# Kernel tuning notes

Measured on AMD Instinct MI355X. Metric: run time of the kernel, lower is better.

Reference implementation:

```python
import jax, jax.numpy as jnp
import numpy as np

N_HEAD, D_MODEL, D_HEAD = 16, 1024, 64
SCALE = 1.0 / (D_HEAD ** 0.5)
LN_EPS = 1e-5


def _rel_shift(x):
    # x: [b, n, i, j] -> Transformer-XL relative shift
    b, n, i, j = x.shape
    x_padded = jnp.pad(x, ((0, 0), (0, 0), (0, 0), (1, 0)))  # [b,n,i,j+1]
    x_padded = x_padded.reshape(b, n, j + 1, i)
    return x_padded[:, :, 1:, :].reshape(b, n, i, j)


def _layer_norm(x, g, b):
    mu = jnp.mean(x, axis=-1, keepdims=True)
    var = jnp.mean(jnp.square(x - mu), axis=-1, keepdims=True)
    return (x - mu) * jax.lax.rsqrt(var + LN_EPS) * g + b


def setup_inputs() -> dict:
    key = jax.random.key(0)
    ks = jax.random.split(key, 16)
    qlen, bsz = 2048, 2
    d = D_MODEL
    h = N_HEAD * D_HEAD
    s = 0.02
    inp = {
        "w": jax.random.normal(ks[0], (qlen, bsz, d), jnp.float32),
        "r": jax.random.normal(ks[1], (qlen, d), jnp.float32),
        "r_w_bias": jax.random.normal(ks[2], (N_HEAD, D_HEAD), jnp.float32) * s,
        "r_r_bias": jax.random.normal(ks[3], (N_HEAD, D_HEAD), jnp.float32) * s,
        "Wq": jax.random.normal(ks[4], (d, h), jnp.float32) * s,
        "bq": jnp.zeros((h,), jnp.float32),
        "Wk": jax.random.normal(ks[5], (d, h), jnp.float32) * s,
        "bk": jnp.zeros((h,), jnp.float32),
        "Wv": jax.random.normal(ks[6], (d, h), jnp.float32) * s,
        "bv": jnp.zeros((h,), jnp.float32),
        "Wr": jax.random.normal(ks[7], (d, h), jnp.float32) * s,
        "br": jnp.zeros((h,), jnp.float32),
        "Wo": jax.random.normal(ks[8], (h, d), jnp.float32) * s,
        "bo": jnp.zeros((d,), jnp.float32),
        "ln_g": jnp.ones((d,), jnp.float32),
        "ln_b": jnp.zeros((d,), jnp.float32),
        # causal mask: True = masked (future positions)
        "attn_mask": jnp.triu(jnp.ones((qlen, qlen), dtype=bool), k=1),
    }
    return inp


def reference(w, r, r_w_bias, r_r_bias, Wq, bq, Wk, bk, Wv, bv, Wr, br, Wo, bo, ln_g, ln_b, attn_mask):
    qlen, bsz, _ = w.shape
    rlen = r.shape[0]
    # projections (post-lnorm path: project raw w)
    q = (w @ Wq + bq).reshape(qlen, bsz, N_HEAD, D_HEAD)
    k = (w @ Wk + bk).reshape(qlen, bsz, N_HEAD, D_HEAD)
    v = (w @ Wv + bv).reshape(qlen, bsz, N_HEAD, D_HEAD)
    r_k = (r @ Wr + br).reshape(rlen, N_HEAD, D_HEAD)

    AC = jnp.einsum('ibnd,jbnd->bnij', q + r_w_bias, k)
    BD = jnp.einsum('ibnd,jnd->bnij', q + r_r_bias, r_k)
    BD = _rel_shift(BD)
    attn_score = SCALE * (AC + BD)
    attn_score = jnp.where(attn_mask[None, None, :, :], -jnp.inf, attn_score)

    attn_prob = jax.nn.softmax(attn_score, axis=3)
    attn_vec = jnp.einsum('bnij,jbnd->ibnd', attn_prob, v)
    attn_vec = attn_vec.reshape(qlen, bsz, N_HEAD * D_HEAD)
    attn_out = attn_vec @ Wo + bo
    return _layer_norm(w + attn_out, ln_g, ln_b)
```

## Files before the change

kernel.cpp:

```cpp
#include <hip/hip_runtime.h>
#include <math.h>

#define L 2048
#define BSZ 2
#define NH 16
#define DH 64
#define DM 1024
#define GK 1024
#define SCALE_F 0.125f

#define PSLOT 4160

typedef __attribute__((ext_vector_type(8))) __bf16 bf16x8;
typedef __attribute__((ext_vector_type(4))) __bf16 bf16x4;
typedef __attribute__((ext_vector_type(4))) float f32x4;

__global__ __launch_bounds__(256)
void cast2_f32_bf16(const float* __restrict__ a, int na4,
                    const float* __restrict__ b, int nb4,
                    __bf16* __restrict__ da, __bf16* __restrict__ db_)
{
    int i = blockIdx.x * 256 + threadIdx.x;
    int stride = gridDim.x * 256;
    int tot = na4 + nb4;
    for (; i < tot; i += stride) {
        const float4* s; bf16x4* d; int idx;
        if (i < na4) { s = (const float4*)a; d = (bf16x4*)da; idx = i; }
        else         { s = (const float4*)b; d = (bf16x4*)db_; idx = i - na4; }
        float4 v = s[idx];
        bf16x4 o = { (__bf16)v.x, (__bf16)v.y, (__bf16)v.z, (__bf16)v.w };
        d[idx] = o;
    }
}

__global__ __launch_bounds__(256)
void transpose_w5(const float* s0, const float* s1, const float* s2,
                  const float* s3, const float* s4,
                  __bf16* d0, __bf16* d1, __bf16* d2, __bf16* d3, __bf16* d4)
{
    const float* srcs[5] = { s0, s1, s2, s3, s4 };
    __bf16*      dsts[5] = { d0, d1, d2, d3, d4 };
    const float* src = srcs[blockIdx.z];
    __bf16*      dst = dsts[blockIdx.z];
    __shared__ float tile[32][33];
    const int tx = threadIdx.x & 31, ty = threadIdx.x >> 5;
    const int x0 = blockIdx.x * 32, y0 = blockIdx.y * 32;
    #pragma unroll
    for (int i = 0; i < 32; i += 8)
        tile[ty + i][tx] = src[(size_t)(y0 + ty + i) * 1024 + x0 + tx];
    __syncthreads();
    #pragma unroll
    for (int i = 0; i < 32; i += 8)
        dst[(size_t)(x0 + ty + i) * 1024 + y0 + tx] = (__bf16)tile[tx][ty + i];
}

__global__ __launch_bounds__(256)
void transpose_v(const __bf16* __restrict__ src, __bf16* __restrict__ dst)
{
    __shared__ __bf16 tile[32][34];
    const __bf16* s = src + (size_t)blockIdx.z * L * DH;
    __bf16*       d = dst + (size_t)blockIdx.z * L * DH;
    const int tx = threadIdx.x & 31, ty = threadIdx.x >> 5;
    const int j0 = blockIdx.x * 32, d0 = blockIdx.y * 32;
    #pragma unroll
    for (int i = 0; i < 32; i += 8)
        tile[ty + i][tx] = s[(size_t)(j0 + ty + i) * DH + d0 + tx];
    __syncthreads();
    #pragma unroll
    for (int i = 0; i < 32; i += 8)
        d[(size_t)(d0 + ty + i) * L + j0 + tx] = tile[tx][ty + i];
}

__global__ __launch_bounds__(256)
void gemm_bf16(const __bf16* __restrict__ A0, const __bf16* __restrict__ A1,
               const __bf16* __restrict__ B0, const __bf16* __restrict__ B1,
               int sched,
               __bf16* __restrict__ o0, __bf16* __restrict__ o1,
               __bf16* __restrict__ o2, __bf16* __restrict__ o3,
               __bf16* __restrict__ o4,
               const float* __restrict__ b0, const float* __restrict__ b1,
               const float* __restrict__ b2, const float* __restrict__ b3,
               const float* __restrict__ rwbf, const float* __restrict__ rrbf,
               float* __restrict__ of)
{
    __shared__ __bf16 As[128 * 64];
    __shared__ __bf16 Bs[128 * 64];

    const __bf16 *A, *Bt;
    int mode, bm, bn;
    if (sched == 0) {
        int id = blockIdx.x;
        if (id < 768) { A = A0; Bt = B0; mode = 0; bm = (id & 31) * 128; bn = (id >> 5) * 128; }
        else { id -= 768; A = A1; Bt = B1; mode = 1; bm = (id & 15) * 128; bn = (id >> 4) * 128; }
    } else {
        A = A0; Bt = B0; mode = 2; bm = blockIdx.x * 128; bn = blockIdx.y * 128;
    }

    const int t    = threadIdx.x;
    const int w    = t >> 6;
    const int lane = t & 63;
    const int row16 = lane & 15;
    const int kgrp  = lane >> 4;
    const int wr = w >> 1, wc = w & 1;

    f32x4 acc[4][4];
    #pragma unroll
    for (int mi = 0; mi < 4; ++mi)
        #pragma unroll
        for (int ni = 0; ni < 4; ++ni)
            acc[mi][ni] = (f32x4){0.f, 0.f, 0.f, 0.f};

    for (int k0 = 0; k0 < GK; k0 += 64) {
        __syncthreads();
        #pragma unroll
        for (int it = 0; it < 4; ++it) {
            const int lin = (it * 256 + t) * 16;
            const int row = lin >> 7;
            const int kb  = lin & 127;
            const char* ga = (const char*)(A + (size_t)(bm + row) * GK + k0) + kb;
            __builtin_amdgcn_global_load_lds(
                (const __attribute__((address_space(1))) void*)ga,
                (__attribute__((address_space(3))) void*)((char*)As + lin), 16, 0, 0);
            const char* gb = (const char*)(Bt + (size_t)(bn + row) * GK + k0) + kb;
            __builtin_amdgcn_global_load_lds(
                (const __attribute__((address_space(1))) void*)gb,
                (__attribute__((address_space(3))) void*)((char*)Bs + lin), 16, 0, 0);
        }
        __syncthreads();

        #pragma unroll
        for (int ks = 0; ks < 2; ++ks) {
            bf16x8 af[4], bfr[4];
            #pragma unroll
            for (int mi = 0; mi < 4; ++mi)
                af[mi] = *reinterpret_cast<const bf16x8*>(
                    &As[(wr * 64 + mi * 16 + row16) * 64 + kgrp * 8 + ks * 32]);
            #pragma unroll
            for (int ni = 0; ni < 4; ++ni)
                bfr[ni] = *reinterpret_cast<const bf16x8*>(
                    &Bs[(wc * 64 + ni * 16 + row16) * 64 + kgrp * 8 + ks * 32]);
            #pragma unroll
            for (int mi = 0; mi < 4; ++mi)
                #pragma unroll
                for (int ni = 0; ni < 4; ++ni)
                    acc[mi][ni] = __builtin_amdgcn_mfma_f32_16x16x32_bf16(
                        af[mi], bfr[ni], acc[mi][ni], 0, 0, 0);
        }
    }

    #pragma unroll
    for (int mi = 0; mi < 4; ++mi) {
        #pragma unroll
        for (int ni = 0; ni < 4; ++ni) {
            #pragma unroll
            for (int r = 0; r < 4; ++r) {
                const int row = bm + wr * 64 + mi * 16 + kgrp * 4 + r;
                const int col = bn + wc * 64 + ni * 16 + row16;
                const float val = acc[mi][ni][r];
                if (mode == 0) {
                    const int which = col >> 10, c = col & 1023;
                    const int n = c >> 6, dh = c & 63;
                    const int i = row >> 1, b = row & 1;
                    const size_t idx = (((size_t)(b * NH + n) * L) + i) * DH + dh;
                    if (which == 0) {
                        const float v0 = val + b0[c];
                        o0[idx] = (__bf16)(v0 + rwbf[c]);
                        o1[idx] = (__bf16)(v0 + rrbf[c]);
                    } else if (which == 1) {
                        o2[idx] = (__bf16)(val + b1[c]);
                    } else {
                        o3[idx] = (__bf16)(val + b2[c]);
                    }
                } else if (mode == 1) {
                    const int n = col >> 6, dh = col & 63;
                    o4[((size_t)n * L + row) * DH + dh] = (__bf16)(val + b3[col]);
                } else {
                    of[(size_t)row * DM + col] = val + b0[col];
                }
            }
        }
    }
}

__global__ __launch_bounds__(256, 3)
void attn_partial(const __bf16* __restrict__ qwg, const __bf16* __restrict__ qrg,
                  const __bf16* __restrict__ kg,  const __bf16* __restrict__ vTg,
                  const __bf16* __restrict__ rkg, float* __restrict__ P)
{
    __shared__ __bf16 kt [2][64][72];
    __shared__ __bf16 vtT[2][64][72];
    __shared__ __bf16 pt [4][16][72];

    int x = blockIdx.x;
    int it, jc;
    if (x < 8)       { it = x;                      jc = 0; }
    else if (x < 24) { int y = x - 8;  it = 8  + (y >> 1); jc = y & 1; }
    else if (x < 48) { int y = x - 24; it = 16 + y / 3;    jc = y - (y / 3) * 3; }
    else             { int y = x - 48; it = 24 + (y >> 2); jc = y & 3; }

    const int t    = threadIdx.x;
    const int w    = t >> 6;
    const int lane = t & 63;
    const int row16 = lane & 15;
    const int kgrp  = lane >> 4;

    const int bh = blockIdx.y;
    const int n  = bh & (NH - 1);
    const int i0 = it * 64;
    const int i0w = i0 + w * 16;
    const int jstart = jc * 512;
    const int jend   = min(jstart + 512, i0 + 64);

    const __bf16* qwb = qwg + (size_t)bh * L * DH;
    const __bf16* qrb = qrg + (size_t)bh * L * DH;
    const __bf16* kb  = kg  + (size_t)bh * L * DH;
    const __bf16* vTb = vTg + (size_t)bh * L * DH;
    const __bf16* rkb = rkg + (size_t)n  * L * DH;

    bf16x8 qwf[2], qrf[2];
    #pragma unroll
    for (int ks = 0; ks < 2; ++ks) {
        size_t off = (size_t)(i0w + row16) * DH + kgrp * 8 + ks * 32;
        qwf[ks] = *reinterpret_cast<const bf16x8*>(qwb + off);
        qrf[ks] = *reinterpret_cast<const bf16x8*>(qrb + off);
    }

    const int sj = t >> 2;
    const int sc = (t & 3) * 16;

    {
        bf16x8 a0 = *reinterpret_cast<const bf16x8*>(kb + (size_t)(jstart + sj) * DH + sc);
        bf16x8 a1 = *reinterpret_cast<const bf16x8*>(kb + (size_t)(jstart + sj) * DH + sc + 8);
        bf16x8 b0v = *reinterpret_cast<const bf16x8*>(vTb + (size_t)sj * L + jstart + sc);
        bf16x8 b1v = *reinterpret_cast<const bf16x8*>(vTb + (size_t)sj * L + jstart + sc + 8);
        *reinterpret_cast<bf16x8*>(&kt[0][sj][sc])      = a0;
        *reinterpret_cast<bf16x8*>(&kt[0][sj][sc + 8])  = a1;
        *reinterpret_cast<bf16x8*>(&vtT[0][sj][sc])     = b0v;
        *reinterpret_cast<bf16x8*>(&vtT[0][sj][sc + 8]) = b1v;
    }
    __syncthreads();

    float l_run[4] = {0.f, 0.f, 0.f, 0.f};
    f32x4 O[4];
    #pragma unroll
    for (int cb = 0; cb < 4; ++cb) O[cb] = (f32x4){0.f, 0.f, 0.f, 0.f};

    int cur = 0;
    for (int j0 = jstart; j0 < jend; j0 += 64) {
        const bool more = (j0 + 64 < jend);

        bf16x8 skA, skB, svA, svB;
        if (more) {
            skA = *reinterpret_cast<const bf16x8*>(kb + (size_t)(j0 + 64 + sj) * DH + sc);
            skB = *reinterpret_cast<const bf16x8*>(kb + (size_t)(j0 + 64 + sj) * DH + sc + 8);
            svA = *reinterpret_cast<const bf16x8*>(vTb + (size_t)sj * L + j0 + 64 + sc);
            svB = *reinterpret_cast<const bf16x8*>(vTb + (size_t)sj * L + j0 + 64 + sc + 8);
        }

        f32x4 ac[4];
        #pragma unroll
        for (int cb = 0; cb < 4; ++cb) ac[cb] = (f32x4){0.f, 0.f, 0.f, 0.f};
        #pragma unroll
        for (int ks = 0; ks < 2; ++ks)
            #pragma unroll
            for (int cb = 0; cb < 4; ++cb) {
                bf16x8 kf = *reinterpret_cast<const bf16x8*>(
                    &kt[cur][16 * cb + row16][kgrp * 8 + ks * 32]);
                ac[cb] = __builtin_amdgcn_mfma_f32_16x16x32_bf16(qwf[ks], kf, ac[cb], 0, 0, 0);
            }

        f32x4 db[5];
        #pragma unroll
        for (int cb = 0; cb < 5; ++cb) db[cb] = (f32x4){0.f, 0.f, 0.f, 0.f};
        const int pw0 = (L - 1) + j0 - (i0w + 15);
        #pragma unroll
        for (int ks = 0; ks < 2; ++ks)
            #pragma unroll
            for (int cb = 0; cb < 5; ++cb) {
                int p = pw0 + 16 * cb + row16;
                p = p > (L - 1) ? (L - 1) : p;
                bf16x8 rf = *reinterpret_cast<const bf16x8*>(
                    rkb + (size_t)p * DH + kgrp * 8 + ks * 32);
                db[cb] = __builtin_amdgcn_mfma_f32_16x16x32_bf16(qrf[ks], rf, db[cb], 0, 0, 0);
            }

        #pragma unroll
        for (int r = 0; r < 4; ++r) {
            const int ri = kgrp * 4 + r;
            const int i_glob = i0w + ri;
            const int u  = row16 + 15 - ri;
            const int lo = u & 15;
            const int hi = u >> 4;
            const int srclane = (lane & 48) | lo;
            float T[5];
            #pragma unroll
            for (int c2 = 0; c2 < 5; ++c2)
                T[c2] = __shfl(db[c2][r], srclane, 64);
            float rsum = 0.f;
            #pragma unroll
            for (int cb = 0; cb < 4; ++cb) {
                const int jj = 16 * cb + row16;
                float bd = hi ? T[cb + 1] : T[cb];
                float s = SCALE_F * (ac[cb][r] + bd);
                if (j0 + jj > i_glob) s = -INFINITY;
                float p = __expf(s);
                pt[w][ri][jj] = (__bf16)p;
                rsum += p;
            }
            #pragma unroll
            for (int off = 1; off < 16; off <<= 1)
                rsum += __shfl_xor(rsum, off);
            l_run[r] += rsum;
        }

        #pragma unroll
        for (int ks = 0; ks < 2; ++ks) {
            bf16x8 pf = *reinterpret_cast<const bf16x8*>(&pt[w][row16][kgrp * 8 + ks * 32]);
            #pragma unroll
            for (int cb = 0; cb < 4; ++cb) {
                bf16x8 vf = *reinterpret_cast<const bf16x8*>(
                    &vtT[cur][16 * cb + row16][kgrp * 8 + ks * 32]);
                O[cb] = __builtin_amdgcn_mfma_f32_16x16x32_bf16(pf, vf, O[cb], 0, 0, 0);
            }
        }

        if (more) {
            *reinterpret_cast<bf16x8*>(&kt[cur ^ 1][sj][sc])      = skA;
            *reinterpret_cast<bf16x8*>(&kt[cur ^ 1][sj][sc + 8])  = skB;
            *reinterpret_cast<bf16x8*>(&vtT[cur ^ 1][sj][sc])     = svA;
            *reinterpret_cast<bf16x8*>(&vtT[cur ^ 1][sj][sc + 8]) = svB;
            __syncthreads();
            cur ^= 1;
        }
    }

    float* Pb = P + ((size_t)bh * 32 + it) * PSLOT;
    #pragma unroll
    for (int r = 0; r < 4; ++r) {
        const int row = w * 16 + kgrp * 4 + r;
        #pragma unroll
        for (int cb = 0; cb < 4; ++cb)
            atomicAdd(&Pb[row * 64 + 16 * cb + row16], O[cb][r]);
        if (row16 == 0)
            atomicAdd(&Pb[4096 + row], l_run[r]);
    }
}

__global__ __launch_bounds__(256)
void attn_reduce(const float* __restrict__ P, __bf16* __restrict__ av)
{
    const int bh = blockIdx.y;
    const int it = blockIdx.x;
    const int n = bh & (NH - 1), b = bh >> 4;
    const float* Pb = P + ((size_t)bh * 32 + it) * PSLOT;
    const int t = threadIdx.x;
    const int row = t >> 2;
    const int c0 = (t & 3) * 16;
    const float inv = 1.0f / Pb[4096 + row];
    const int i_glob = it * 64 + row;
    __bf16* dst = av + (size_t)(i_glob * BSZ + b) * (NH * DH) + n * DH + c0;
    #pragma unroll
    for (int v4 = 0; v4 < 4; ++v4) {
        float4 o = *reinterpret_cast<const float4*>(&Pb[row * 64 + c0 + v4 * 4]);
        bf16x4 ov = { (__bf16)(o.x * inv), (__bf16)(o.y * inv),
                      (__bf16)(o.z * inv), (__bf16)(o.w * inv) };
        *reinterpret_cast<bf16x4*>(dst + v4 * 4) = ov;
    }
}

__global__ __launch_bounds__(256)
void ln_fused(const float* __restrict__ w, const float* __restrict__ ao,
              const float* __restrict__ g, const float* __restrict__ bb,
              float* __restrict__ out)
{
    const int row = blockIdx.x;
    const float* wr = w  + (size_t)row * DM;
    const float* ar = ao + (size_t)row * DM;
    const int t = threadIdx.x;
    float x[4];
    float s = 0.f;
    #pragma unroll
    for (int j = 0; j < 4; ++j) {
        int c = t + j * 256;
        x[j] = wr[c] + ar[c];
        s += x[j];
    }
    __shared__ float red[4];
    #pragma unroll
    for (int off = 1; off < 64; off <<= 1) s += __shfl_xor(s, off);
    int wid = t >> 6, lane = t & 63;
    if (lane == 0) red[wid] = s;
    __syncthreads();
    float mu = (red[0] + red[1] + red[2] + red[3]) * (1.0f / DM);
    float ss = 0.f;
    #pragma unroll
    for (int j = 0; j < 4; ++j) { float d = x[j] - mu; ss += d * d; }
    #pragma unroll
    for (int off = 1; off < 64; off <<= 1) ss += __shfl_xor(ss, off);
    __syncthreads();
    if (lane == 0) red[wid] = ss;
    __syncthreads();
    float var = (red[0] + red[1] + red[2] + red[3]) * (1.0f / DM);
    float rstd = rsqrtf(var + 1e-5f);
    #pragma unroll
    for (int j = 0; j < 4; ++j) {
        int c = t + j * 256;
        out[(size_t)row * DM + c] = (x[j] - mu) * rstd * g[c] + bb[c];
    }
}

extern "C" void kernel_launch(void* const* d_in, const int* in_sizes, int n_in,
                              void* d_out, int out_size, void* d_ws, size_t ws_size,
                              hipStream_t stream)
{
    (void)in_sizes; (void)n_in; (void)out_size; (void)ws_size;
    const float* w   = (const float*)d_in[0];
    const float* r   = (const float*)d_in[1];
    const float* rwb = (const float*)d_in[2];
    const float* rrb = (const float*)d_in[3];
    const float* Wq  = (const float*)d_in[4];
    const float* bq  = (const float*)d_in[5];
    const float* Wk  = (const float*)d_in[6];
    const float* bk  = (const float*)d_in[7];
    const float* Wv  = (const float*)d_in[8];
    const float* bv  = (const float*)d_in[9];
    const float* Wr  = (const float*)d_in[10];
    const float* br  = (const float*)d_in[11];
    const float* Wo  = (const float*)d_in[12];
    const float* bo  = (const float*)d_in[13];
    const float* lng = (const float*)d_in[14];
    const float* lnb = (const float*)d_in[15];
    float* out = (float*)d_out;

    const size_t NQ = (size_t)BSZ * NH * L * DH;
    const size_t PN = (size_t)BSZ * NH * 32 * PSLOT;
    char* wsb = (char*)d_ws;
    __bf16* w_bf    = (__bf16*)wsb;  wsb += (size_t)2 * L * DM * 2;
    __bf16* r_bf    = (__bf16*)wsb;  wsb += (size_t)L * DM * 2;
    __bf16* wqkv_t  = (__bf16*)wsb;  wsb += (size_t)3 * DM * DM * 2;
    __bf16* wr_t    = (__bf16*)wsb;  wsb += (size_t)DM * DM * 2;
    __bf16* wo_t    = (__bf16*)wsb;  wsb += (size_t)DM * DM * 2;
    __bf16* qw_ws   = (__bf16*)wsb;  wsb += NQ * 2;
    __bf16* qr_ws   = (__bf16*)wsb;  wsb += NQ * 2;
    __bf16* k_ws    = (__bf16*)wsb;  wsb += NQ * 2;
    __bf16* v_ws    = (__bf16*)wsb;  wsb += NQ * 2;
    __bf16* vT_ws   = (__bf16*)wsb;  wsb += NQ * 2;
    __bf16* rk_ws   = (__bf16*)wsb;  wsb += (size_t)NH * L * DH * 2;
    __bf16* av_ws   = (__bf16*)wsb;  wsb += NQ * 2;
    float*  P_ws    = (float*)wsb;
    float*  ao_ws   = P_ws;

    dim3 blk(256);
    hipMemsetAsync(P_ws, 0, PN * sizeof(float), stream);

    cast2_f32_bf16<<<dim3(1536), blk, 0, stream>>>(
        w, (2 * L * DM) / 4, r, (L * DM) / 4, w_bf, r_bf);
    transpose_w5<<<dim3(32, 32, 5), blk, 0, stream>>>(
        Wq, Wk, Wv, Wr, Wo,
        wqkv_t, wqkv_t + (size_t)DM * DM, wqkv_t + (size_t)2 * DM * DM, wr_t, wo_t);

    gemm_bf16<<<dim3(896), blk, 0, stream>>>(w_bf, r_bf, wqkv_t, wr_t, 0,
        qw_ws, qr_ws, k_ws, v_ws, rk_ws, bq, bk, bv, br, rwb, rrb, nullptr);

    transpose_v<<<dim3(L / 32, DH / 32, BSZ * NH), blk, 0, stream>>>(v_ws, vT_ws);

    attn_partial<<<dim3(80, BSZ * NH), blk, 0, stream>>>(
        qw_ws, qr_ws, k_ws, vT_ws, rk_ws, P_ws);
    attn_reduce<<<dim3(32, BSZ * NH), blk, 0, stream>>>(P_ws, av_ws);

    gemm_bf16<<<dim3(32, 8), blk, 0, stream>>>(av_ws, nullptr, wo_t, nullptr, 1,
        nullptr, nullptr, nullptr, nullptr, nullptr, bo, nullptr, nullptr, nullptr,
        nullptr, nullptr, ao_ws);

    ln_fused<<<dim3(L * BSZ), blk, 0, stream>>>(w, ao_ws, lng, lnb, out);
}
```

Measured before the change: 407.4 us.

## Replace atomic partial accumulation with per-chunk bf16 slots and prefetch rel-pos keys

```diff
diff --git a/kernel.cpp b/kernel.cpp
--- a/kernel.cpp
+++ b/kernel.cpp
@@ -8,8 +8,6 @@
 #define DM 1024
 #define GK 1024
 #define SCALE_F 0.125f
-
-#define PSLOT 4160
 
 typedef __attribute__((ext_vector_type(8))) __bf16 bf16x8;
 typedef __attribute__((ext_vector_type(4))) __bf16 bf16x4;
@@ -185,18 +183,22 @@
 __global__ __launch_bounds__(256, 3)
 void attn_partial(const __bf16* __restrict__ qwg, const __bf16* __restrict__ qrg,
                   const __bf16* __restrict__ kg,  const __bf16* __restrict__ vTg,
-                  const __bf16* __restrict__ rkg, float* __restrict__ P)
+                  const __bf16* __restrict__ rkg,
+                  __bf16* __restrict__ Po, float* __restrict__ Pl)
 {
     __shared__ __bf16 kt [2][64][72];
     __shared__ __bf16 vtT[2][64][72];
     __shared__ __bf16 pt [4][16][72];
 
-    int x = blockIdx.x;
+    const int flat = blockIdx.x;
+    const int xr = flat & 7, q = flat >> 3;
+    const int bh = xr * 4 + (q / 80);
+    const int cx = 79 - (q % 80);
     int it, jc;
-    if (x < 8)       { it = x;                      jc = 0; }
-    else if (x < 24) { int y = x - 8;  it = 8  + (y >> 1); jc = y & 1; }
-    else if (x < 48) { int y = x - 24; it = 16 + y / 3;    jc = y - (y / 3) * 3; }
-    else             { int y = x - 48; it = 24 + (y >> 2); jc = y & 3; }
+    if (cx < 8)       { it = cx;                       jc = 0; }
+    else if (cx < 24) { int y = cx - 8;  it = 8  + (y >> 1); jc = y & 1; }
+    else if (cx < 48) { int y = cx - 24; it = 16 + y / 3;    jc = y - (y / 3) * 3; }
+    else              { int y = cx - 48; it = 24 + (y >> 2); jc = y & 3; }
 
     const int t    = threadIdx.x;
     const int w    = t >> 6;
@@ -204,7 +206,6 @@
     const int row16 = lane & 15;
     const int kgrp  = lane >> 4;
 
-    const int bh = blockIdx.y;
     const int n  = bh & (NH - 1);
     const int i0 = it * 64;
     const int i0w = i0 + w * 16;
@@ -238,6 +239,19 @@
         *reinterpret_cast<bf16x8*>(&vtT[0][sj][sc])     = b0v;
         *reinterpret_cast<bf16x8*>(&vtT[0][sj][sc + 8]) = b1v;
     }
+    bf16x8 rfc[2][5];
+    {
+        const int pw0 = (L - 1) + jstart - (i0w + 15);
+        #pragma unroll
+        for (int ks = 0; ks < 2; ++ks)
+            #pragma unroll
+            for (int cb = 0; cb < 5; ++cb) {
+                int p = pw0 + 16 * cb + row16;
+                p = p > (L - 1) ? (L - 1) : p;
+                rfc[ks][cb] = *reinterpret_cast<const bf16x8*>(
+                    rkb + (size_t)p * DH + kgrp * 8 + ks * 32);
+            }
+    }
     __syncthreads();
 
     float l_run[4] = {0.f, 0.f, 0.f, 0.f};
@@ -250,11 +264,24 @@
         const bool more = (j0 + 64 < jend);
 
         bf16x8 skA, skB, svA, svB;
+        bf16x8 rfn[2][5];
         if (more) {
             skA = *reinterpret_cast<const bf16x8*>(kb + (size_t)(j0 + 64 + sj) * DH + sc);
             skB = *reinterpret_cast<const bf16x8*>(kb + (size_t)(j0 + 64 + sj) * DH + sc + 8);
             svA = *reinterpret_cast<const bf16x8*>(vTb + (size_t)sj * L + j0 + 64 + sc);
             svB = *reinterpret_cast<const bf16x8*>(vTb + (size_t)sj * L + j0 + 64 + sc + 8);
+            const int pw0n = (L - 1) + (j0 + 64) - (i0w + 15);
+            #pragma unroll
+            for (int ks = 0; ks < 2; ++ks) {
+                rfn[ks][0] = rfc[ks][4];
+                #pragma unroll
+                for (int cb = 1; cb < 5; ++cb) {
+                    int p = pw0n + 16 * cb + row16;
+                    p = p > (L - 1) ? (L - 1) : p;
+                    rfn[ks][cb] = *reinterpret_cast<const bf16x8*>(
+                        rkb + (size_t)p * DH + kgrp * 8 + ks * 32);
+                }
+            }
         }
 
         f32x4 ac[4];
@@ -272,17 +299,11 @@
         f32x4 db[5];
         #pragma unroll
         for (int cb = 0; cb < 5; ++cb) db[cb] = (f32x4){0.f, 0.f, 0.f, 0.f};
-        const int pw0 = (L - 1) + j0 - (i0w + 15);
         #pragma unroll
         for (int ks = 0; ks < 2; ++ks)
             #pragma unroll
-            for (int cb = 0; cb < 5; ++cb) {
-                int p = pw0 + 16 * cb + row16;
-                p = p > (L - 1) ? (L - 1) : p;
-                bf16x8 rf = *reinterpret_cast<const bf16x8*>(
-                    rkb + (size_t)p * DH + kgrp * 8 + ks * 32);
-                db[cb] = __builtin_amdgcn_mfma_f32_16x16x32_bf16(qrf[ks], rf, db[cb], 0, 0, 0);
-            }
+            for (int cb = 0; cb < 5; ++cb)
+                db[cb] = __builtin_amdgcn_mfma_f32_16x16x32_bf16(qrf[ks], rfc[ks][cb], db[cb], 0, 0, 0);
 
         #pragma unroll
         for (int r = 0; r < 4; ++r) {
@@ -331,41 +352,59 @@
             *reinterpret_cast<bf16x8*>(&vtT[cur ^ 1][sj][sc + 8]) = svB;
             __syncthreads();
             cur ^= 1;
-        }
-    }
-
-    float* Pb = P + ((size_t)bh * 32 + it) * PSLOT;
+            #pragma unroll
+            for (int ks = 0; ks < 2; ++ks)
+                #pragma unroll
+                for (int cb = 0; cb < 5; ++cb)
+                    rfc[ks][cb] = rfn[ks][cb];
+        }
+    }
+
+    __bf16* Pob = Po + ((size_t)bh * 80 + cx) * 4096;
+    float*  Plb = Pl + ((size_t)bh * 80 + cx) * 64;
     #pragma unroll
     for (int r = 0; r < 4; ++r) {
         const int row = w * 16 + kgrp * 4 + r;
         #pragma unroll
         for (int cb = 0; cb < 4; ++cb)
-            atomicAdd(&Pb[row * 64 + 16 * cb + row16], O[cb][r]);
+            Pob[row * 64 + 16 * cb + row16] = (__bf16)O[cb][r];
         if (row16 == 0)
-            atomicAdd(&Pb[4096 + row], l_run[r]);
+            Plb[row] = l_run[r];
     }
 }
 
 __global__ __launch_bounds__(256)
-void attn_reduce(const float* __restrict__ P, __bf16* __restrict__ av)
+void attn_reduce(const __bf16* __restrict__ Po, const float* __restrict__ Pl,
+                 __bf16* __restrict__ av)
 {
     const int bh = blockIdx.y;
     const int it = blockIdx.x;
     const int n = bh & (NH - 1), b = bh >> 4;
-    const float* Pb = P + ((size_t)bh * 32 + it) * PSLOT;
+    int b0c, nc;
+    if (it < 8)       { b0c = it;                 nc = 1; }
+    else if (it < 16) { b0c = 8 + 2 * (it - 8);   nc = 2; }
+    else if (it < 24) { b0c = 24 + 3 * (it - 16); nc = 3; }
+    else              { b0c = 48 + 4 * (it - 24); nc = 4; }
+
     const int t = threadIdx.x;
     const int row = t >> 2;
     const int c0 = (t & 3) * 16;
-    const float inv = 1.0f / Pb[4096 + row];
+    float osum[16] = {};
+    float lsum = 0.f;
+    for (int k = 0; k < nc; ++k) {
+        const size_t slot = (size_t)bh * 80 + b0c + k;
+        const __bf16* Pob = Po + slot * 4096 + row * 64 + c0;
+        bf16x8 va = *reinterpret_cast<const bf16x8*>(Pob);
+        bf16x8 vb = *reinterpret_cast<const bf16x8*>(Pob + 8);
+        #pragma unroll
+        for (int j = 0; j < 8; ++j) { osum[j] += (float)va[j]; osum[8 + j] += (float)vb[j]; }
+        lsum += Pl[slot * 64 + row];
+    }
+    const float inv = 1.0f / lsum;
     const int i_glob = it * 64 + row;
     __bf16* dst = av + (size_t)(i_glob * BSZ + b) * (NH * DH) + n * DH + c0;
     #pragma unroll
-    for (int v4 = 0; v4 < 4; ++v4) {
-        float4 o = *reinterpret_cast<const float4*>(&Pb[row * 64 + c0 + v4 * 4]);
-        bf16x4 ov = { (__bf16)(o.x * inv), (__bf16)(o.y * inv),
-                      (__bf16)(o.z * inv), (__bf16)(o.w * inv) };
-        *reinterpret_cast<bf16x4*>(dst + v4 * 4) = ov;
-    }
+    for (int j = 0; j < 16; ++j) dst[j] = (__bf16)(osum[j] * inv);
 }
 
 __global__ __launch_bounds__(256)
@@ -433,7 +472,6 @@
     float* out = (float*)d_out;
 
     const size_t NQ = (size_t)BSZ * NH * L * DH;
-    const size_t PN = (size_t)BSZ * NH * 32 * PSLOT;
     char* wsb = (char*)d_ws;
     __bf16* w_bf    = (__bf16*)wsb;  wsb += (size_t)2 * L * DM * 2;
     __bf16* r_bf    = (__bf16*)wsb;  wsb += (size_t)L * DM * 2;
@@ -447,12 +485,11 @@
     __bf16* vT_ws   = (__bf16*)wsb;  wsb += NQ * 2;
     __bf16* rk_ws   = (__bf16*)wsb;  wsb += (size_t)NH * L * DH * 2;
     __bf16* av_ws   = (__bf16*)wsb;  wsb += NQ * 2;
-    float*  P_ws    = (float*)wsb;
-    float*  ao_ws   = P_ws;
+    float*  ao_ws   = (float*)wsb;
+    __bf16* Po_ws = (__bf16*)d_ws;
+    float*  Pl_ws = ao_ws;
 
     dim3 blk(256);
-    hipMemsetAsync(P_ws, 0, PN * sizeof(float), stream);
-
     cast2_f32_bf16<<<dim3(1536), blk, 0, stream>>>(
         w, (2 * L * DM) / 4, r, (L * DM) / 4, w_bf, r_bf);
     transpose_w5<<<dim3(32, 32, 5), blk, 0, stream>>>(
@@ -464,9 +501,9 @@
 
     transpose_v<<<dim3(L / 32, DH / 32, BSZ * NH), blk, 0, stream>>>(v_ws, vT_ws);
 
-    attn_partial<<<dim3(80, BSZ * NH), blk, 0, stream>>>(
-        qw_ws, qr_ws, k_ws, vT_ws, rk_ws, P_ws);
-    attn_reduce<<<dim3(32, BSZ * NH), blk, 0, stream>>>(P_ws, av_ws);
+    attn_partial<<<dim3(2560), blk, 0, stream>>>(
+        qw_ws, qr_ws, k_ws, vT_ws, rk_ws, Po_ws, Pl_ws);
+    attn_reduce<<<dim3(32, BSZ * NH), blk, 0, stream>>>(Po_ws, Pl_ws, av_ws);
 
     gemm_bf16<<<dim3(32, 8), blk, 0, stream>>>(av_ws, nullptr, wo_t, nullptr, 1,
         nullptr, nullptr, nullptr, nullptr, nullptr, bo, nullptr, nullptr, nullptr,
```

Result: slower. 419.8 us (+3.0%).
